# Performance work log

Hardware: AMD Instinct MI355X
Metric: run time of the kernel (lower is better)

Reference implementation:

```python
import jax, jax.numpy as jnp
import numpy as np

DIM = 1024
HEADS = 16
HEAD_DIM = DIM // HEADS
SCALE = HEAD_DIM ** -0.5


def setup_inputs() -> dict:
    key = jax.random.key(0)
    ks = jax.random.split(key, 7)
    B, N, M = 2, 2048, 2048
    x = jax.random.normal(ks[0], (B, N, DIM), dtype=jnp.float32)
    y = jax.random.normal(ks[1], (B, M, DIM), dtype=jnp.float32)
    s = DIM ** -0.5
    Wq = jax.random.normal(ks[2], (DIM, DIM), dtype=jnp.float32) * s
    Wk = jax.random.normal(ks[3], (DIM, DIM), dtype=jnp.float32) * s
    Wv = jax.random.normal(ks[4], (DIM, DIM), dtype=jnp.float32) * s
    Wp = jax.random.normal(ks[5], (DIM, DIM), dtype=jnp.float32) * s
    bp = jax.random.normal(ks[6], (DIM,), dtype=jnp.float32) * 0.01
    return {"x": x, "y": y, "Wq": Wq, "Wk": Wk, "Wv": Wv, "Wp": Wp, "bp": bp}


def _split_heads(t):
    b, n, _ = t.shape
    return t.reshape(b, n, HEADS, HEAD_DIM).transpose(0, 2, 1, 3)  # b h n d


def reference(x, y, Wq, Wk, Wv, Wp, bp):
    q = _split_heads(x @ Wq)  # [b,h,n,d]
    k = _split_heads(y @ Wk)  # [b,h,m,d]
    v = _split_heads(y @ Wv)  # [b,h,m,d]
    attn = jnp.einsum('bhid,bhjd->bhij', q, k) * SCALE  # [b,h,n,m]
    attn = jax.nn.softmax(attn, axis=-1)
    out = jnp.einsum('bhij,bhjd->bhid', attn, v)  # [b,h,n,d]
    b, h, n, d = out.shape
    out = out.transpose(0, 2, 1, 3).reshape(b, n, h * d)  # [b,n,dim]
    return out @ Wp + bp
```

## Files before the change

kernel.cpp:

```cpp
#include <hip/hip_runtime.h>
#include <hip/hip_bf16.h>
#include <cstdint>

#define DIM   1024
#define HEADS 16
#define HDIM  64
#define BATCH 2
#define SEQ   2048
#define ROWS  (BATCH*SEQ)
static constexpr float QSCALE = 0.18033688f;

typedef float  f32x4  __attribute__((ext_vector_type(4)));
typedef float  float4v __attribute__((ext_vector_type(4)));
typedef __bf16 bf16x8 __attribute__((ext_vector_type(8)));
typedef __bf16 bf16x4 __attribute__((ext_vector_type(4)));

__device__ __forceinline__ void glds16(const __bf16* g, __bf16* l) {
  __builtin_amdgcn_global_load_lds(
      (const __attribute__((address_space(1))) void*)g,
      (__attribute__((address_space(3))) void*)l, 16, 0, 0);
}

__global__ __launch_bounds__(256) void cvt_kernel(const float* __restrict__ x,
                                                  const float* __restrict__ y,
                                                  __bf16* __restrict__ xb,
                                                  __bf16* __restrict__ yb, int n4) {
  const int i = blockIdx.x * 256 + threadIdx.x;
  if (i >= n4) return;
  const float* s = blockIdx.y ? y : x;
  __bf16* d = blockIdx.y ? yb : xb;
  const float4v v = *(const float4v*)&s[(size_t)i * 4];
  bf16x4 o;
  o[0] = (__bf16)v[0]; o[1] = (__bf16)v[1]; o[2] = (__bf16)v[2]; o[3] = (__bf16)v[3];
  *(bf16x4*)&d[(size_t)i * 4] = o;
}

__global__ __launch_bounds__(256) void wtrans_kernel(
    const float* __restrict__ Wq, const float* __restrict__ Wk,
    const float* __restrict__ Wv, const float* __restrict__ Wp,
    __bf16* __restrict__ Wt) {
  const int z = blockIdx.z;
  const float* W = (z == 0) ? Wq : (z == 1) ? Wk : (z == 2) ? Wv : Wp;
  __bf16* dst = Wt + (size_t)z * DIM * DIM;
  __shared__ float T[64][65];
  const int t = threadIdx.x;
  const int n0 = blockIdx.x * 64, k0 = blockIdx.y * 64;
  const int col = t & 63, rw = t >> 6;
  #pragma unroll
  for (int p = 0; p < 16; ++p) {
    const int row = p * 4 + rw;
    T[row][col] = W[(size_t)(k0 + row) * DIM + n0 + col];
  }
  __syncthreads();
  #pragma unroll
  for (int p = 0; p < 16; ++p) {
    const int row = p * 4 + rw;
    dst[(size_t)(n0 + row) * DIM + k0 + col] = (__bf16)T[col][row];
  }
}

__global__ __launch_bounds__(256) void proj_kernel(
    const __bf16* __restrict__ xb, const __bf16* __restrict__ yb,
    const __bf16* __restrict__ Wt,
    __bf16* __restrict__ Qb, __bf16* __restrict__ Kb, __bf16* __restrict__ VT) {
  const int z = blockIdx.z;
  const __bf16* A = (z == 0) ? xb : yb;
  const __bf16* B = Wt + (size_t)z * DIM * DIM;

  __shared__ __bf16 As[128 * 64];
  __shared__ __bf16 Bs[128 * 64];

  const int t = threadIdx.x, lane = t & 63, wave = t >> 6;
  const int l15 = lane & 15, quad = lane >> 4;
  const int wm = wave & 1, wn = wave >> 1;
  const int rowBase = blockIdx.y * 128, colBase = blockIdx.x * 128;
  const int srow = lane >> 3;
  const int scol = ((lane & 7) ^ srow) * 8;

  f32x4 acc[4][4] = {};

  for (int kb = 0; kb < DIM; kb += 64) {
    __syncthreads();
    #pragma unroll
    for (int i = 0; i < 4; ++i) {
      const int c = wave * 4 + i;
      const int row = c * 8 + srow;
      glds16(&A[(size_t)(rowBase + row) * DIM + kb + scol], &As[c * 512]);
      glds16(&B[(size_t)(colBase + row) * DIM + kb + scol], &Bs[c * 512]);
    }
    __syncthreads();
    #pragma unroll
    for (int ks = 0; ks < 2; ++ks) {
      bf16x8 a[4], b[4];
      #pragma unroll
      for (int mi = 0; mi < 4; ++mi) {
        const int row = wm * 64 + mi * 16 + l15;
        a[mi] = *(const bf16x8*)&As[row * 64 + (((ks << 2) | quad) ^ (row & 7)) * 8];
      }
      #pragma unroll
      for (int ni = 0; ni < 4; ++ni) {
        const int row = wn * 64 + ni * 16 + l15;
        b[ni] = *(const bf16x8*)&Bs[row * 64 + (((ks << 2) | quad) ^ (row & 7)) * 8];
      }
      #pragma unroll
      for (int mi = 0; mi < 4; ++mi)
        #pragma unroll
        for (int ni = 0; ni < 4; ++ni)
          acc[mi][ni] = __builtin_amdgcn_mfma_f32_16x16x32_bf16(a[mi], b[ni], acc[mi][ni], 0, 0, 0);
    }
  }

  if (z < 2) {
    __bf16* out = (z == 0) ? Qb : Kb;
    const float sc = (z == 0) ? QSCALE : 1.0f;
    #pragma unroll
    for (int mi = 0; mi < 4; ++mi) {
      const int row0 = rowBase + wm * 64 + mi * 16 + quad * 4;
      #pragma unroll
      for (int ni = 0; ni < 4; ++ni) {
        const int col = colBase + wn * 64 + ni * 16 + l15;
        #pragma unroll
        for (int r = 0; r < 4; ++r)
          out[(size_t)(row0 + r) * DIM + col] = (__bf16)(acc[mi][ni][r] * sc);
      }
    }
  } else {
    #pragma unroll
    for (int mi = 0; mi < 4; ++mi) {
      const int row0 = rowBase + wm * 64 + mi * 16 + quad * 4;
      const int bb = row0 >> 11, key0 = row0 & (SEQ - 1);
      #pragma unroll
      for (int ni = 0; ni < 4; ++ni) {
        const int col = colBase + wn * 64 + ni * 16 + l15;
        const int h = col >> 6, d = col & 63;
        bf16x4 pk;
        #pragma unroll
        for (int r = 0; r < 4; ++r) pk[r] = (__bf16)acc[mi][ni][r];
        *(bf16x4*)&VT[((size_t)((bb * HEADS + h) * HDIM + d)) * SEQ + key0] = pk;
      }
    }
  }
}

__global__ __launch_bounds__(256) void attn_kernel(
    const __bf16* __restrict__ Qb, const __bf16* __restrict__ Kb,
    const __bf16* __restrict__ VT, __bf16* __restrict__ Ob) {
  __shared__ __bf16 Ks[64 * 64];
  __shared__ __bf16 Vs[64 * 64];
  __shared__ __bf16 Ps[4][32][72];

  const int t = threadIdx.x, lane = t & 63, wave = t >> 6;
  const int l15 = lane & 15, quad = lane >> 4;
  const int bh = blockIdx.y, b = bh >> 4, h = bh & 15;
  const int qrow0 = blockIdx.x * 128 + wave * 32;
  const int srow = lane >> 3;
  const int scol = ((lane & 7) ^ srow) * 8;

  bf16x8 qf[2][2];
  #pragma unroll
  for (int mi = 0; mi < 2; ++mi)
    #pragma unroll
    for (int ks = 0; ks < 2; ++ks)
      qf[mi][ks] = *(const bf16x8*)&Qb[(size_t)(b * SEQ + qrow0 + mi * 16 + l15) * DIM
                                       + h * HDIM + ks * 32 + quad * 8];

  bf16x8 ones;
  #pragma unroll
  for (int i = 0; i < 8; ++i) ones[i] = (__bf16)1.0f;

  f32x4 o[2][4] = {};
  f32x4 lacc[2] = {};

  const __bf16* Kbh = Kb + (size_t)b * SEQ * DIM + h * HDIM;
  const __bf16* Vbh = VT + (size_t)bh * HDIM * SEQ;

  for (int jb = 0; jb < SEQ; jb += 64) {
    __syncthreads();
    #pragma unroll
    for (int i = 0; i < 2; ++i) {
      const int c = wave * 2 + i;
      const int row = c * 8 + srow;
      glds16(&Kbh[(size_t)(jb + row) * DIM + scol], &Ks[c * 512]);
      glds16(&Vbh[(size_t)row * SEQ + jb + scol], &Vs[c * 512]);
    }
    __syncthreads();

    f32x4 sT[4][2] = {};
    #pragma unroll
    for (int ks = 0; ks < 2; ++ks) {
      #pragma unroll
      for (int ni = 0; ni < 4; ++ni) {
        const int row = ni * 16 + l15;
        const bf16x8 kf = *(const bf16x8*)&Ks[row * 64 + (((ks << 2) | quad) ^ (row & 7)) * 8];
        #pragma unroll
        for (int mi = 0; mi < 2; ++mi)
          sT[ni][mi] = __builtin_amdgcn_mfma_f32_16x16x32_bf16(kf, qf[mi][ks], sT[ni][mi], 0, 0, 0);
      }
    }

    #pragma unroll
    for (int ni = 0; ni < 4; ++ni)
      #pragma unroll
      for (int mi = 0; mi < 2; ++mi) {
        bf16x4 pk;
        #pragma unroll
        for (int r = 0; r < 4; ++r)
          pk[r] = (__bf16)__builtin_amdgcn_exp2f(sT[ni][mi][r]);
        *(bf16x4*)&Ps[wave][mi * 16 + l15][ni * 16 + quad * 4] = pk;
      }

    #pragma unroll
    for (int ks = 0; ks < 2; ++ks) {
      bf16x8 pa[2];
      #pragma unroll
      for (int mi = 0; mi < 2; ++mi)
        pa[mi] = *(const bf16x8*)&Ps[wave][mi * 16 + l15][ks * 32 + quad * 8];
      #pragma unroll
      for (int mi = 0; mi < 2; ++mi)
        lacc[mi] = __builtin_amdgcn_mfma_f32_16x16x32_bf16(pa[mi], ones, lacc[mi], 0, 0, 0);
      #pragma unroll
      for (int dt = 0; dt < 4; ++dt) {
        const int row = dt * 16 + l15;
        const bf16x8 vf = *(const bf16x8*)&Vs[row * 64 + (((ks << 2) | quad) ^ (row & 7)) * 8];
        #pragma unroll
        for (int mi = 0; mi < 2; ++mi)
          o[mi][dt] = __builtin_amdgcn_mfma_f32_16x16x32_bf16(pa[mi], vf, o[mi][dt], 0, 0, 0);
      }
    }
  }

  #pragma unroll
  for (int mi = 0; mi < 2; ++mi)
    #pragma unroll
    for (int r = 0; r < 4; ++r) {
      const float inv = 1.f / lacc[mi][r];
      const int row = b * SEQ + qrow0 + mi * 16 + quad * 4 + r;
      #pragma unroll
      for (int dt = 0; dt < 4; ++dt)
        Ob[(size_t)row * DIM + h * HDIM + dt * 16 + l15] = (__bf16)(o[mi][dt][r] * inv);
    }
}

__global__ __launch_bounds__(256) void outproj_kernel(
    const __bf16* __restrict__ A, const __bf16* __restrict__ Bt,
    const float* __restrict__ bias, float* __restrict__ out) {
  __shared__ __bf16 As[128 * 64];
  __shared__ __bf16 Bs[128 * 64];

  const int t = threadIdx.x, lane = t & 63, wave = t >> 6;
  const int l15 = lane & 15, quad = lane >> 4;
  const int wm = wave & 1, wn = wave >> 1;
  const int rowBase = blockIdx.y * 128, colBase = blockIdx.x * 128;
  const int srow = lane >> 3;
  const int scol = ((lane & 7) ^ srow) * 8;

  f32x4 acc[4][4] = {};

  for (int kb = 0; kb < DIM; kb += 64) {
    __syncthreads();
    #pragma unroll
    for (int i = 0; i < 4; ++i) {
      const int c = wave * 4 + i;
      const int row = c * 8 + srow;
      glds16(&A[(size_t)(rowBase + row) * DIM + kb + scol], &As[c * 512]);
      glds16(&Bt[(size_t)(colBase + row) * DIM + kb + scol], &Bs[c * 512]);
    }
    __syncthreads();
    #pragma unroll
    for (int ks = 0; ks < 2; ++ks) {
      bf16x8 a[4], b[4];
      #pragma unroll
      for (int mi = 0; mi < 4; ++mi) {
        const int row = wm * 64 + mi * 16 + l15;
        a[mi] = *(const bf16x8*)&As[row * 64 + (((ks << 2) | quad) ^ (row & 7)) * 8];
      }
      #pragma unroll
      for (int ni = 0; ni < 4; ++ni) {
        const int row = wn * 64 + ni * 16 + l15;
        b[ni] = *(const bf16x8*)&Bs[row * 64 + (((ks << 2) | quad) ^ (row & 7)) * 8];
      }
      #pragma unroll
      for (int mi = 0; mi < 4; ++mi)
        #pragma unroll
        for (int ni = 0; ni < 4; ++ni)
          acc[mi][ni] = __builtin_amdgcn_mfma_f32_16x16x32_bf16(a[mi], b[ni], acc[mi][ni], 0, 0, 0);
    }
  }

  #pragma unroll
  for (int mi = 0; mi < 4; ++mi) {
    const int row0 = rowBase + wm * 64 + mi * 16 + quad * 4;
    #pragma unroll
    for (int ni = 0; ni < 4; ++ni) {
      const int col = colBase + wn * 64 + ni * 16 + l15;
      const float bb = bias[col];
      #pragma unroll
      for (int r = 0; r < 4; ++r)
        out[(size_t)(row0 + r) * DIM + col] = acc[mi][ni][r] + bb;
    }
  }
}

extern "C" void kernel_launch(void* const* d_in, const int* in_sizes, int n_in,
                              void* d_out, int out_size, void* d_ws, size_t ws_size,
                              hipStream_t stream) {
  const float* x  = (const float*)d_in[0];
  const float* y  = (const float*)d_in[1];
  const float* Wq = (const float*)d_in[2];
  const float* Wk = (const float*)d_in[3];
  const float* Wv = (const float*)d_in[4];
  const float* Wp = (const float*)d_in[5];
  const float* bp = (const float*)d_in[6];
  float* out = (float*)d_out;

  const size_t NEL = (size_t)ROWS * DIM;
  __bf16* xb = (__bf16*)d_ws;
  __bf16* yb = xb + NEL;
  __bf16* Wt = yb + NEL;
  __bf16* Qb = Wt + NEL;
  __bf16* Kb = Qb + NEL;
  __bf16* VT = Kb + NEL;
  __bf16* Ob = VT + NEL;

  cvt_kernel<<<dim3(NEL / 4 / 256, 2), 256, 0, stream>>>(x, y, xb, yb, NEL / 4);
  wtrans_kernel<<<dim3(16, 16, 4), 256, 0, stream>>>(Wq, Wk, Wv, Wp, Wt);
  proj_kernel<<<dim3(DIM / 128, ROWS / 128, 3), 256, 0, stream>>>(xb, yb, Wt, Qb, Kb, VT);
  attn_kernel<<<dim3(SEQ / 128, BATCH * HEADS), 256, 0, stream>>>(Qb, Kb, VT, Ob);
  outproj_kernel<<<dim3(DIM / 128, ROWS / 128), 256, 0, stream>>>(Ob, Wt + 3 * (size_t)DIM * DIM, bp, out);
}
```

Measured before the change: 223.8 us.

## Double-buffer K/V tiles and split keys across waves in attention kernel

The attention kernel now double-buffers K/V tiles in LDS, issuing the async load of the next tile before computing on the current one, so one barrier per iteration replaces two. Each wave handles 64 query rows and half of each 64-key tile instead of 32 rows and the full tile, which lets each K/V fragment load feed more MFMAs. The two key-halves are reduced through LDS at the end. The P scratch layout is changed to a padded transposed layout, and launch bounds request two blocks per CU. The costs are higher register pressure from 4x4 accumulators and a final cross-wave reduction step.

```diff
diff --git a/kernel.cpp b/kernel.cpp
--- a/kernel.cpp
+++ b/kernel.cpp
@@ -142,23 +142,26 @@
   }
 }
 
-__global__ __launch_bounds__(256) void attn_kernel(
+__global__ __launch_bounds__(256, 2) void attn_kernel(
     const __bf16* __restrict__ Qb, const __bf16* __restrict__ Kb,
     const __bf16* __restrict__ VT, __bf16* __restrict__ Ob) {
-  __shared__ __bf16 Ks[64 * 64];
-  __shared__ __bf16 Vs[64 * 64];
-  __shared__ __bf16 Ps[4][32][72];
+  __shared__ __bf16 KV[2][2][64 * 64];
+  __shared__ __bf16 Ps[4][2080];
 
   const int t = threadIdx.x, lane = t & 63, wave = t >> 6;
   const int l15 = lane & 15, quad = lane >> 4;
   const int bh = blockIdx.y, b = bh >> 4, h = bh & 15;
-  const int qrow0 = blockIdx.x * 128 + wave * 32;
+  const int qseg = wave & 1, kh = wave >> 1;
+  const int qrow0 = blockIdx.x * 128 + qseg * 64;
   const int srow = lane >> 3;
   const int scol = ((lane & 7) ^ srow) * 8;
 
-  bf16x8 qf[2][2];
-  #pragma unroll
-  for (int mi = 0; mi < 2; ++mi)
+  const __bf16* Kbh = Kb + (size_t)b * SEQ * DIM + h * HDIM;
+  const __bf16* Vbh = VT + (size_t)bh * HDIM * SEQ;
+
+  bf16x8 qf[4][2];
+  #pragma unroll
+  for (int mi = 0; mi < 4; ++mi)
     #pragma unroll
     for (int ks = 0; ks < 2; ++ks)
       qf[mi][ks] = *(const bf16x8*)&Qb[(size_t)(b * SEQ + qrow0 + mi * 16 + l15) * DIM
@@ -168,77 +171,100 @@
   #pragma unroll
   for (int i = 0; i < 8; ++i) ones[i] = (__bf16)1.0f;
 
-  f32x4 o[2][4] = {};
-  f32x4 lacc[2] = {};
-
-  const __bf16* Kbh = Kb + (size_t)b * SEQ * DIM + h * HDIM;
-  const __bf16* Vbh = VT + (size_t)bh * HDIM * SEQ;
-
-  for (int jb = 0; jb < SEQ; jb += 64) {
-    __syncthreads();
+  f32x4 o[4][4] = {};
+  f32x4 lacc[4] = {};
+
+  auto stage = [&](int jb, int buf) {
     #pragma unroll
     for (int i = 0; i < 2; ++i) {
       const int c = wave * 2 + i;
       const int row = c * 8 + srow;
-      glds16(&Kbh[(size_t)(jb + row) * DIM + scol], &Ks[c * 512]);
-      glds16(&Vbh[(size_t)row * SEQ + jb + scol], &Vs[c * 512]);
-    }
-    __syncthreads();
-
-    f32x4 sT[4][2] = {};
-    #pragma unroll
-    for (int ks = 0; ks < 2; ++ks) {
-      #pragma unroll
-      for (int ni = 0; ni < 4; ++ni) {
-        const int row = ni * 16 + l15;
-        const bf16x8 kf = *(const bf16x8*)&Ks[row * 64 + (((ks << 2) | quad) ^ (row & 7)) * 8];
-        #pragma unroll
-        for (int mi = 0; mi < 2; ++mi)
+      glds16(&Kbh[(size_t)(jb + row) * DIM + scol], &KV[buf][0][c * 512]);
+      glds16(&Vbh[(size_t)row * SEQ + jb + scol], &KV[buf][1][c * 512]);
+    }
+  };
+
+  stage(0, 0);
+  for (int j = 0; j < SEQ / 64; ++j) {
+    const int buf = j & 1;
+    __syncthreads();
+    if (j + 1 < SEQ / 64) stage((j + 1) * 64, buf ^ 1);
+    const __bf16* Ks = KV[buf][0];
+    const __bf16* Vs = KV[buf][1];
+
+    f32x4 sT[2][4] = {};
+    #pragma unroll
+    for (int ks = 0; ks < 2; ++ks)
+      #pragma unroll
+      for (int ni = 0; ni < 2; ++ni) {
+        const int key = kh * 32 + ni * 16 + l15;
+        const bf16x8 kf = *(const bf16x8*)&Ks[key * 64 + (((ks << 2) | quad) ^ (key & 7)) * 8];
+        #pragma unroll
+        for (int mi = 0; mi < 4; ++mi)
           sT[ni][mi] = __builtin_amdgcn_mfma_f32_16x16x32_bf16(kf, qf[mi][ks], sT[ni][mi], 0, 0, 0);
       }
-    }
-
-    #pragma unroll
-    for (int ni = 0; ni < 4; ++ni)
-      #pragma unroll
-      for (int mi = 0; mi < 2; ++mi) {
+
+    #pragma unroll
+    for (int ni = 0; ni < 2; ++ni)
+      #pragma unroll
+      for (int mi = 0; mi < 4; ++mi) {
         bf16x4 pk;
         #pragma unroll
         for (int r = 0; r < 4; ++r)
           pk[r] = (__bf16)__builtin_amdgcn_exp2f(sT[ni][mi][r]);
-        *(bf16x4*)&Ps[wave][mi * 16 + l15][ni * 16 + quad * 4] = pk;
-      }
-
-    #pragma unroll
-    for (int ks = 0; ks < 2; ++ks) {
-      bf16x8 pa[2];
-      #pragma unroll
-      for (int mi = 0; mi < 2; ++mi)
-        pa[mi] = *(const bf16x8*)&Ps[wave][mi * 16 + l15][ks * 32 + quad * 8];
-      #pragma unroll
-      for (int mi = 0; mi < 2; ++mi)
-        lacc[mi] = __builtin_amdgcn_mfma_f32_16x16x32_bf16(pa[mi], ones, lacc[mi], 0, 0, 0);
-      #pragma unroll
-      for (int dt = 0; dt < 4; ++dt) {
-        const int row = dt * 16 + l15;
-        const bf16x8 vf = *(const bf16x8*)&Vs[row * 64 + (((ks << 2) | quad) ^ (row & 7)) * 8];
-        #pragma unroll
-        for (int mi = 0; mi < 2; ++mi)
-          o[mi][dt] = __builtin_amdgcn_mfma_f32_16x16x32_bf16(pa[mi], vf, o[mi][dt], 0, 0, 0);
-      }
-    }
-  }
-
-  #pragma unroll
-  for (int mi = 0; mi < 2; ++mi)
-    #pragma unroll
-    for (int r = 0; r < 4; ++r) {
-      const float inv = 1.f / lacc[mi][r];
-      const int row = b * SEQ + qrow0 + mi * 16 + quad * 4 + r;
-      #pragma unroll
-      for (int dt = 0; dt < 4; ++dt)
-        Ob[(size_t)row * DIM + h * HDIM + dt * 16 + l15] = (__bf16)(o[mi][dt][r] * inv);
-    }
+        *(bf16x4*)&Ps[wave][((ni * 4 + quad) * 65 + mi * 16 + l15) * 4] = pk;
+      }
+
+    bf16x8 pa[4];
+    #pragma unroll
+    for (int mi = 0; mi < 4; ++mi) {
+      const bf16x4 plo = *(const bf16x4*)&Ps[wave][((2 * quad) * 65 + mi * 16 + l15) * 4];
+      const bf16x4 phi = *(const bf16x4*)&Ps[wave][((2 * quad + 1) * 65 + mi * 16 + l15) * 4];
+      #pragma unroll
+      for (int r = 0; r < 4; ++r) { pa[mi][r] = plo[r]; pa[mi][4 + r] = phi[r]; }
+      lacc[mi] = __builtin_amdgcn_mfma_f32_16x16x32_bf16(pa[mi], ones, lacc[mi], 0, 0, 0);
+    }
+    #pragma unroll
+    for (int dt = 0; dt < 4; ++dt) {
+      const int d = dt * 16 + l15;
+      const bf16x8 vf = *(const bf16x8*)&Vs[d * 64 + (((kh << 2) | quad) ^ (d & 7)) * 8];
+      #pragma unroll
+      for (int mi = 0; mi < 4; ++mi)
+        o[mi][dt] = __builtin_amdgcn_mfma_f32_16x16x32_bf16(pa[mi], vf, o[mi][dt], 0, 0, 0);
+    }
+  }
+
+  __syncthreads();
+  float* mb = (float*)&KV[0][0][0];
+  float* lb = (float*)&Ps[0][0];
+  if (kh == 1) {
+    #pragma unroll
+    for (int mi = 0; mi < 4; ++mi)
+      #pragma unroll
+      for (int r = 0; r < 4; ++r) {
+        const int q = mi * 16 + quad * 4 + r;
+        #pragma unroll
+        for (int dt = 0; dt < 4; ++dt)
+          mb[qseg * 4096 + q * 64 + dt * 16 + l15] = o[mi][dt][r];
+        if (l15 == 0) lb[qseg * 64 + q] = lacc[mi][r];
+      }
+  }
+  __syncthreads();
+  if (kh == 0) {
+    #pragma unroll
+    for (int mi = 0; mi < 4; ++mi)
+      #pragma unroll
+      for (int r = 0; r < 4; ++r) {
+        const int q = mi * 16 + quad * 4 + r;
+        const float inv = 1.f / (lacc[mi][r] + lb[qseg * 64 + q]);
+        const size_t row = (size_t)(b * SEQ + qrow0 + q);
+        #pragma unroll
+        for (int dt = 0; dt < 4; ++dt) {
+          const float ov = o[mi][dt][r] + mb[qseg * 4096 + q * 64 + dt * 16 + l15];
+          Ob[row * DIM + h * HDIM + dt * 16 + l15] = (__bf16)(ov * inv);
+        }
+      }
+  }
 }
 
 __global__ __launch_bounds__(256) void outproj_kernel(
```

New measurement: 220.0 us. No clear change (-1.7%).
